# Kernel optimization log

Hardware: AMD Instinct MI355X
Metric: run time of the kernel (lower is better)

Reference implementation:

```python
import jax, jax.numpy as jnp
import numpy as np
import math

B, S, E, H, F, L, V = 4, 256, 512, 8, 2048, 4, 32000
HD = E // H
MAXLEN = 5000  # EnhancedPositionalEncoding max_len default


def _ln(x, s, b):
    m = jnp.mean(x, axis=-1, keepdims=True)
    v = jnp.mean((x - m) ** 2, axis=-1, keepdims=True)
    return (x - m) / jnp.sqrt(v + 1e-5) * s + b


def setup_inputs() -> dict:
    key = jax.random.key(0)
    ks = jax.random.split(key, 10)
    n = lambda k, shape: jax.random.normal(k, shape, jnp.float32) * 0.02
    return {
        "src": jax.random.randint(ks[0], (B, S), 0, V),
        "emb": jax.random.uniform(ks[1], (V, E), jnp.float32, -0.1, 0.1),
        "rel_table": n(ks[2], (2 * MAXLEN - 1, E)),
        "norm_in_s": jnp.ones(E, jnp.float32), "norm_in_b": jnp.zeros(E, jnp.float32),
        "inW": n(ks[3], (L, 3 * E, E)), "inB": jnp.zeros((L, 3 * E), jnp.float32),
        "outW": n(ks[4], (L, E, E)), "outB": jnp.zeros((L, E), jnp.float32),
        "ln1_s": jnp.ones((L, E), jnp.float32), "ln1_b": jnp.zeros((L, E), jnp.float32),
        "ln2_s": jnp.ones((L, E), jnp.float32), "ln2_b": jnp.zeros((L, E), jnp.float32),
        "w1": n(ks[5], (L, F, E)), "b1": jnp.zeros((L, F), jnp.float32),
        "w2": n(ks[6], (L, E, F)), "b2": jnp.zeros((L, E), jnp.float32),
        "normf_s": jnp.ones(E, jnp.float32), "normf_b": jnp.zeros(E, jnp.float32),
        "dec_w": jax.random.uniform(ks[7], (V, E), jnp.float32, -0.1, 0.1),
        "dec_b": jnp.zeros(V, jnp.float32),
    }


def reference(src, emb, rel_table, norm_in_s, norm_in_b, inW, inB, outW, outB,
              ln1_s, ln1_b, ln2_s, ln2_b, w1, b1, w2, b2, normf_s, normf_b,
              dec_w, dec_b):
    x = emb[src] * math.sqrt(E)                 # [B,S,E], pos_encoder is identity in relative mode
    x = _ln(x, norm_in_s, norm_in_b)
    # relative-position embedding gather: idx[l,m] = (m - l) + S - 1
    pos = jnp.arange(S)
    rel_idx = (pos[None, :] - pos[:, None]) + S - 1
    rel = rel_table[rel_idx].reshape(S, S, H, HD)  # [S,S,H,hd]
    # NOTE: torch adds the BOOL triu mask to float scores -> +1.0 at masked positions
    mask = jnp.triu(jnp.ones((S, S), jnp.float32), 1)
    scale = 1.0 / math.sqrt(HD)
    for l in range(L):
        h = _ln(x, ln1_s[l], ln1_b[l])
        qkv = h @ inW[l].T + inB[l]
        q, k, v = jnp.split(qkv, 3, axis=-1)
        q = q.reshape(B, S, H, HD).transpose(0, 2, 1, 3)  # [B,H,S,hd]
        k = k.reshape(B, S, H, HD).transpose(0, 2, 1, 3)
        v = v.reshape(B, S, H, HD).transpose(0, 2, 1, 3)
        scores = jnp.einsum('bhqd,bhkd->bhqk', q, k) * scale
        bias = jnp.einsum('bhld,lmhd->bhlm', q, rel)      # relative-position bias (unscaled, as in torch)
        attn = jax.nn.softmax(scores + bias + mask, axis=-1)
        o = jnp.einsum('bhqk,bhkd->bhqd', attn, v).transpose(0, 2, 1, 3).reshape(B, S, E)
        x = x + (o @ outW[l].T + outB[l])
        h2 = _ln(x, ln2_s[l], ln2_b[l])
        ff = jax.nn.gelu(h2 @ w1[l].T + b1[l], approximate=False) @ w2[l].T + b2[l]
        x = x + ff
    x = _ln(x, normf_s, normf_b)  # encoder final norm
    return x @ dec_w.T + dec_b    # [B,S,V]
```

## Files before the change

### kernel.cpp

```cpp
#include <hip/hip_runtime.h>
#include <hip/hip_bf16.h>
#include <math.h>

#define BB 4
#define SS 256
#define EE 512
#define HH 8
#define HD 64
#define FFD 2048
#define LL 4
#define VV 32000
#define BS (BB*SS)
#define SQRT_E 22.627416997969522f
#define ATTN_SCALE 0.125f

typedef __bf16 bf16;
typedef __attribute__((ext_vector_type(4))) __bf16 bf16x4;
typedef __attribute__((ext_vector_type(8))) __bf16 bf16x8;
typedef __attribute__((ext_vector_type(4))) float f32x4;

#define GLOBAL_AS __attribute__((address_space(1)))
#define LDS_AS    __attribute__((address_space(3)))

__device__ __forceinline__ void load_lds16(const bf16* g, bf16* l) {
    __builtin_amdgcn_global_load_lds((const GLOBAL_AS unsigned int*)g,
                                     (LDS_AS unsigned int*)l, 16, 0, 0);
}

__global__ void cvt_all(const float* __restrict__ inW, const float* __restrict__ outW,
                        const float* __restrict__ w1, const float* __restrict__ w2,
                        const float* __restrict__ dec, const float* __restrict__ rel,
                        bf16* __restrict__ inWb, bf16* __restrict__ outWb,
                        bf16* __restrict__ w1b, bf16* __restrict__ w2b,
                        bf16* __restrict__ decb, bf16* __restrict__ relb) {
    int b = blockIdx.x;
    const float* s; bf16* d; int base; int n;
    if (b < 3072)       { s = inW;  d = inWb;  base = b;         n = 3145728; }
    else if (b < 4096)  { s = outW; d = outWb; base = b - 3072;  n = 1048576; }
    else if (b < 8192)  { s = w1;   d = w1b;   base = b - 4096;  n = 4194304; }
    else if (b < 12288) { s = w2;   d = w2b;   base = b - 8192;  n = 4194304; }
    else if (b < 28288) { s = dec;  d = decb;  base = b - 12288; n = 16384000; }
    else                { s = rel;  d = relb;  base = b - 28288; n = 261632; }
    int i = (base * 256 + threadIdx.x) * 4;
    if (i < n) {
        float4 v = *(const float4*)(s + i);
        bf16x4 o;
        o[0] = (bf16)v.x; o[1] = (bf16)v.y; o[2] = (bf16)v.z; o[3] = (bf16)v.w;
        *(bf16x4*)(d + i) = o;
    }
}

template <typename OT>
__global__ void ln_kernel(const float* __restrict__ in, const float* __restrict__ sc,
                          const float* __restrict__ bi, OT* __restrict__ out) {
    int row = blockIdx.x;
    int t = threadIdx.x;
    const float* r = in + (size_t)row * EE;
    float v0 = r[t], v1 = r[t + 256];
    float sum = v0 + v1, sq = v0 * v0 + v1 * v1;
    #pragma unroll
    for (int off = 32; off; off >>= 1) {
        sum += __shfl_xor(sum, off);
        sq  += __shfl_xor(sq, off);
    }
    __shared__ float ssum[4], ssq[4];
    int wid = t >> 6, lane = t & 63;
    if (lane == 0) { ssum[wid] = sum; ssq[wid] = sq; }
    __syncthreads();
    sum = ssum[0] + ssum[1] + ssum[2] + ssum[3];
    sq  = ssq[0] + ssq[1] + ssq[2] + ssq[3];
    float mean = sum * (1.0f / EE);
    float var  = sq * (1.0f / EE) - mean * mean;
    float rstd = rsqrtf(var + 1e-5f);
    out[(size_t)row * EE + t]       = (OT)((v0 - mean) * rstd * sc[t] + bi[t]);
    out[(size_t)row * EE + t + 256] = (OT)((v1 - mean) * rstd * sc[t + 256] + bi[t + 256]);
}

__global__ void embed_ln_kernel(const int* __restrict__ src, const float* __restrict__ emb,
                                const float* __restrict__ sc, const float* __restrict__ bi,
                                float* __restrict__ out) {
    int row = blockIdx.x;
    int t = threadIdx.x;
    const float* r = emb + (size_t)src[row] * EE;
    float v0 = r[t] * SQRT_E, v1 = r[t + 256] * SQRT_E;
    float sum = v0 + v1, sq = v0 * v0 + v1 * v1;
    #pragma unroll
    for (int off = 32; off; off >>= 1) {
        sum += __shfl_xor(sum, off);
        sq  += __shfl_xor(sq, off);
    }
    __shared__ float ssum[4], ssq[4];
    int wid = t >> 6, lane = t & 63;
    if (lane == 0) { ssum[wid] = sum; ssq[wid] = sq; }
    __syncthreads();
    sum = ssum[0] + ssum[1] + ssum[2] + ssum[3];
    sq  = ssq[0] + ssq[1] + ssq[2] + ssq[3];
    float mean = sum * (1.0f / EE);
    float var  = sq * (1.0f / EE) - mean * mean;
    float rstd = rsqrtf(var + 1e-5f);
    out[(size_t)row * EE + t]       = (v0 - mean) * rstd * sc[t] + bi[t];
    out[(size_t)row * EE + t + 256] = (v1 - mean) * rstd * sc[t + 256] + bi[t + 256];
}

template <int BM, int BN, int MODE, int OBF16, int WRVT, int SWZ>
__global__ __launch_bounds__(256) void gemm_bf16(
        const bf16* __restrict__ A, const bf16* __restrict__ W,
        const float* __restrict__ bias, void* __restrict__ Cout,
        const float* __restrict__ res, bf16* __restrict__ vT,
        int M, int N, int K) {
    constexpr int FM = BM / 32, FN = BN / 32;
    __shared__ bf16 Atile[2][BM * 32];
    __shared__ bf16 Btile[2][BN * 32];
    int tid = threadIdx.x;
    int wid = tid >> 6, lane = tid & 63;
    int wm = (wid >> 1) * (BM / 2), wn = (wid & 1) * (BN / 2);
    int bm, bn;
    if (SWZ) {
        int nbm = gridDim.x;
        int linear = blockIdx.y * nbm + blockIdx.x;
        int total = nbm * gridDim.y;
        int chunk = total >> 3;
        int xcd = linear & 7, idx = linear >> 3;
        int g = xcd * chunk + idx;
        bm = (g % nbm) * BM;
        bn = (g / nbm) * BN;
    } else {
        bm = blockIdx.x * BM;
        bn = blockIdx.y * BN;
    }

    f32x4 acc[FM][FN];
    #pragma unroll
    for (int i = 0; i < FM; i++)
        #pragma unroll
        for (int j = 0; j < FN; j++)
            acc[i][j] = (f32x4){0.f, 0.f, 0.f, 0.f};

    int mrow = lane & 15, kq = (lane >> 4) * 8;

    auto stage = [&](int buf, int k0) {
        #pragma unroll
        for (int it = 0; it < BM / 64; it++) {
            int c = it * 256 + tid;
            int row = c >> 2, kc = (c & 3) * 8;
            load_lds16(A + (size_t)(bm + row) * K + k0 + kc, &Atile[buf][c * 8]);
        }
        #pragma unroll
        for (int it = 0; it < BN / 64; it++) {
            int c = it * 256 + tid;
            int row = c >> 2, kc = (c & 3) * 8;
            load_lds16(W + (size_t)(bn + row) * K + k0 + kc, &Btile[buf][c * 8]);
        }
    };

    stage(0, 0);
    __syncthreads();
    int cur = 0;
    for (int k0 = 0; k0 < K; k0 += 32) {
        if (k0 + 32 < K) stage(cur ^ 1, k0 + 32);
        bf16x8 af[FM], bfv[FN];
        #pragma unroll
        for (int i = 0; i < FM; i++)
            af[i] = *(const bf16x8*)(&Atile[cur][(wm + i * 16 + mrow) * 32 + kq]);
        #pragma unroll
        for (int j = 0; j < FN; j++)
            bfv[j] = *(const bf16x8*)(&Btile[cur][(wn + j * 16 + mrow) * 32 + kq]);
        #pragma unroll
        for (int i = 0; i < FM; i++)
            #pragma unroll
            for (int j = 0; j < FN; j++)
                acc[i][j] = __builtin_amdgcn_mfma_f32_16x16x32_bf16(af[i], bfv[j], acc[i][j], 0, 0, 0);
        __syncthreads();
        cur ^= 1;
    }

    #pragma unroll
    for (int i = 0; i < FM; i++) {
        int row0 = bm + wm + i * 16 + (lane >> 4) * 4;
        #pragma unroll
        for (int j = 0; j < FN; j++) {
            int col = bn + wn + j * 16 + (lane & 15);
            float bv = bias[col];
            #pragma unroll
            for (int r = 0; r < 4; r++) {
                int row = row0 + r;
                float v = acc[i][j][r] + bv;
                if (MODE == 1) v = 0.5f * v * (1.0f + erff(v * 0.7071067811865476f));
                if (MODE == 2) v += res[(size_t)row * N + col];
                if (WRVT && col >= 1024) {
                    int cc = col - 1024;
                    vT[(size_t)(((row >> 8) * 8 + (cc >> 6)) * 64 + (cc & 63)) * 256 + (row & 255)] = (bf16)v;
                } else if (OBF16) ((bf16*)Cout)[(size_t)row * N + col] = (bf16)v;
                else              ((float*)Cout)[(size_t)row * N + col] = v;
            }
        }
    }
}

__global__ __launch_bounds__(256) void attn_mfma(const bf16* __restrict__ qkv,
        const bf16* __restrict__ relb, const bf16* __restrict__ vT,
        bf16* __restrict__ o) {
    int blk = blockIdx.x;
    int qt = blk & 3, bh = blk >> 2;
    int h = bh & 7, b = bh >> 3;
    int q0 = qt * 64, j0 = 192 - q0;
    int tid = threadIdx.x;
    int wid = tid >> 6, lane = tid & 63;
    int l15 = lane & 15, quad = lane >> 4;
    int mr0 = wid * 16;

    __shared__ __align__(16) bf16 Qs[64 * 72];
    __shared__ __align__(16) bf16 Stg[64 * 72];
    __shared__ __align__(16) bf16 BP[64 * 264];

    int c0 = tid, c1 = 256 + tid;
    int r0 = c0 >> 3, ch0 = (c0 & 7) * 8;
    int r1 = c1 >> 3, ch1 = (c1 & 7) * 8;

    const size_t qbase = (size_t)(b * 256 + q0) * 1536 + h * 64;
    *(bf16x8*)(Qs + r0 * 72 + ch0) = *(const bf16x8*)(qkv + qbase + (size_t)r0 * 1536 + ch0);
    *(bf16x8*)(Qs + r1 * 72 + ch1) = *(const bf16x8*)(qkv + qbase + (size_t)r1 * 1536 + ch1);

    bf16x8 pf0, pf1;
    {
        const size_t rb = (size_t)j0 * 512 + h * 64;
        pf0 = *(const bf16x8*)(relb + rb + (size_t)r0 * 512 + ch0);
        pf1 = *(const bf16x8*)(relb + rb + (size_t)r1 * 512 + ch1);
    }

    __syncthreads();
    bf16x8 af0 = *(const bf16x8*)(Qs + (mr0 + l15) * 72 + quad * 8);
    bf16x8 af1 = *(const bf16x8*)(Qs + (mr0 + l15) * 72 + 32 + quad * 8);

    f32x4 S[16];
    #pragma unroll
    for (int i = 0; i < 16; i++) S[i] = (f32x4){0.f, 0.f, 0.f, 0.f};

    for (int jc = 0; jc < 5; jc++) {
        *(bf16x8*)(Stg + r0 * 72 + ch0) = pf0;
        *(bf16x8*)(Stg + r1 * 72 + ch1) = pf1;
        __syncthreads();
        if (jc < 4) {
            const size_t rb = (size_t)(j0 + (jc + 1) * 64) * 512 + h * 64;
            pf0 = *(const bf16x8*)(relb + rb + (size_t)r0 * 512 + ch0);
            pf1 = *(const bf16x8*)(relb + rb + (size_t)r1 * 512 + ch1);
        } else {
            const size_t kb = (size_t)(b * 256) * 1536 + 512 + h * 64;
            pf0 = *(const bf16x8*)(qkv + kb + (size_t)r0 * 1536 + ch0);
            pf1 = *(const bf16x8*)(qkv + kb + (size_t)r1 * 1536 + ch1);
        }
        #pragma unroll
        for (int jt = 0; jt < 4; jt++) {
            f32x4 acc = (f32x4){0.f, 0.f, 0.f, 0.f};
            bf16x8 bv0 = *(const bf16x8*)(Stg + (jt * 16 + l15) * 72 + quad * 8);
            bf16x8 bv1 = *(const bf16x8*)(Stg + (jt * 16 + l15) * 72 + 32 + quad * 8);
            acc = __builtin_amdgcn_mfma_f32_16x16x32_bf16(af0, bv0, acc, 0, 0, 0);
            acc = __builtin_amdgcn_mfma_f32_16x16x32_bf16(af1, bv1, acc, 0, 0, 0);
            int jp = jc * 64 + jt * 16 + l15;
            #pragma unroll
            for (int r = 0; r < 4; r++) {
                int ll = mr0 + quad * 4 + r;
                int m = jp + ll - 63;
                if (m >= 0 && m < 256) BP[ll * 256 + m] = (bf16)acc[r];
            }
        }
        __syncthreads();
    }

    for (int kc = 0; kc < 4; kc++) {
        *(bf16x8*)(Stg + r0 * 72 + ch0) = pf0;
        *(bf16x8*)(Stg + r1 * 72 + ch1) = pf1;
        __syncthreads();
        if (kc < 3) {
            const size_t kb = (size_t)(b * 256 + (kc + 1) * 64) * 1536 + 512 + h * 64;
            pf0 = *(const bf16x8*)(qkv + kb + (size_t)r0 * 1536 + ch0);
            pf1 = *(const bf16x8*)(qkv + kb + (size_t)r1 * 1536 + ch1);
        } else {
            const size_t vb = (size_t)(bh * 64) * 256;
            pf0 = *(const bf16x8*)(vT + vb + (size_t)r0 * 256 + ch0);
            pf1 = *(const bf16x8*)(vT + vb + (size_t)r1 * 256 + ch1);
        }
        #pragma unroll
        for (int nt = 0; nt < 4; nt++) {
            bf16x8 bv0 = *(const bf16x8*)(Stg + (nt * 16 + l15) * 72 + quad * 8);
            bf16x8 bv1 = *(const bf16x8*)(Stg + (nt * 16 + l15) * 72 + 32 + quad * 8);
            S[kc * 4 + nt] = __builtin_amdgcn_mfma_f32_16x16x32_bf16(af0, bv0, S[kc * 4 + nt], 0, 0, 0);
            S[kc * 4 + nt] = __builtin_amdgcn_mfma_f32_16x16x32_bf16(af1, bv1, S[kc * 4 + nt], 0, 0, 0);
        }
        __syncthreads();
    }

    float rmax[4] = {-1e30f, -1e30f, -1e30f, -1e30f};
    #pragma unroll
    for (int T = 0; T < 16; T++) {
        int m = T * 16 + l15;
        #pragma unroll
        for (int r = 0; r < 4; r++) {
            int ll = mr0 + quad * 4 + r;
            float v = S[T][r] * ATTN_SCALE + (float)BP[ll * 256 + m]
                      + ((m > q0 + ll) ? 1.0f : 0.0f);
            S[T][r] = v;
            rmax[r] = fmaxf(rmax[r], v);
        }
    }
    #pragma unroll
    for (int r = 0; r < 4; r++)
        #pragma unroll
        for (int d = 1; d < 16; d <<= 1)
            rmax[r] = fmaxf(rmax[r], __shfl_xor(rmax[r], d));
    float rsum[4] = {0.f, 0.f, 0.f, 0.f};
    #pragma unroll
    for (int T = 0; T < 16; T++)
        #pragma unroll
        for (int r = 0; r < 4; r++) {
            float p = expf(S[T][r] - rmax[r]);
            S[T][r] = p;
            rsum[r] += p;
        }
    #pragma unroll
    for (int r = 0; r < 4; r++)
        #pragma unroll
        for (int d = 1; d < 16; d <<= 1)
            rsum[r] += __shfl_xor(rsum[r], d);

    __syncthreads();
    #pragma unroll
    for (int T = 0; T < 16; T++)
        #pragma unroll
        for (int r = 0; r < 4; r++)
            BP[(mr0 + quad * 4 + r) * 264 + T * 16 + l15] = (bf16)S[T][r];

    f32x4 oacc[4];
    #pragma unroll
    for (int i = 0; i < 4; i++) oacc[i] = (f32x4){0.f, 0.f, 0.f, 0.f};
    for (int kc = 0; kc < 4; kc++) {
        *(bf16x8*)(Stg + r0 * 72 + ch0) = pf0;
        *(bf16x8*)(Stg + r1 * 72 + ch1) = pf1;
        __syncthreads();
        if (kc < 3) {
            const size_t vb = (size_t)(bh * 64) * 256 + (kc + 1) * 64;
            pf0 = *(const bf16x8*)(vT + vb + (size_t)r0 * 256 + ch0);
            pf1 = *(const bf16x8*)(vT + vb + (size_t)r1 * 256 + ch1);
        }
        #pragma unroll
        for (int ks = 0; ks < 2; ks++) {
            bf16x8 ap = *(const bf16x8*)(BP + (mr0 + l15) * 264 + kc * 64 + ks * 32 + quad * 8);
            #pragma unroll
            for (int nt = 0; nt < 4; nt++) {
                bf16x8 bv = *(const bf16x8*)(Stg + (nt * 16 + l15) * 72 + ks * 32 + quad * 8);
                oacc[nt] = __builtin_amdgcn_mfma_f32_16x16x32_bf16(ap, bv, oacc[nt], 0, 0, 0);
            }
        }
        __syncthreads();
    }

    #pragma unroll
    for (int nt = 0; nt < 4; nt++)
        #pragma unroll
        for (int r = 0; r < 4; r++) {
            int ll = mr0 + quad * 4 + r;
            o[(size_t)(b * 256 + q0 + ll) * 512 + h * 64 + nt * 16 + l15] =
                (bf16)(oacc[nt][r] * (1.0f / rsum[r]));
        }
}

template <int MODE>
__global__ void gemm_nt(const float* __restrict__ A, const float* __restrict__ W,
                        const float* __restrict__ bias, float* __restrict__ C,
                        const float* __restrict__ res, int M, int N, int K) {
    __shared__ float As[64][17];
    __shared__ float Ws[64][17];
    int tid = threadIdx.x;
    int tx = tid & 15, ty = tid >> 4;
    int bm = blockIdx.y * 64, bn = blockIdx.x * 64;
    float acc[4][4] = {};
    for (int k0 = 0; k0 < K; k0 += 16) {
        #pragma unroll
        for (int i = 0; i < 4; i++) {
            int idx = tid + i * 256;
            int r = idx >> 4, c = idx & 15;
            As[r][c] = A[(size_t)(bm + r) * K + k0 + c];
            Ws[r][c] = W[(size_t)(bn + r) * K + k0 + c];
        }
        __syncthreads();
        #pragma unroll
        for (int kk = 0; kk < 16; kk++) {
            float a[4], w[4];
            #pragma unroll
            for (int i = 0; i < 4; i++) a[i] = As[ty * 4 + i][kk];
            #pragma unroll
            for (int j = 0; j < 4; j++) w[j] = Ws[tx * 4 + j][kk];
            #pragma unroll
            for (int i = 0; i < 4; i++)
                #pragma unroll
                for (int j = 0; j < 4; j++)
                    acc[i][j] += a[i] * w[j];
        }
        __syncthreads();
    }
    #pragma unroll
    for (int i = 0; i < 4; i++) {
        int row = bm + ty * 4 + i;
        #pragma unroll
        for (int j = 0; j < 4; j++) {
            int col = bn + tx * 4 + j;
            float v = acc[i][j] + bias[col];
            if (MODE == 1) v = 0.5f * v * (1.0f + erff(v * 0.7071067811865476f));
            if (MODE == 2) v += res[(size_t)row * N + col];
            C[(size_t)row * N + col] = v;
        }
    }
}

__global__ void attn_kernel(const float* __restrict__ qkv, const float* __restrict__ rel_table,
                            float* __restrict__ o) {
    int blk = blockIdx.x;
    int l = blk & (SS - 1);
    int bh = blk >> 8;
    int h = bh & (HH - 1);
    int b = bh >> 3;
    int t = threadIdx.x;
    int wid = t >> 6, lane = t & 63;

    __shared__ float qs[HD];
    __shared__ float attn_s[SS];
    __shared__ float swave[4];
    __shared__ float opart[4][HD];

    const float* qrow = qkv + (size_t)(b * SS + l) * (3 * EE) + h * HD;
    if (t < HD) qs[t] = qrow[t];
    __syncthreads();

    const float* krow   = qkv + (size_t)(b * SS + t) * (3 * EE) + EE + h * HD;
    const float* relrow = rel_table + (size_t)(t - l + SS - 1) * EE + h * HD;
    const float4* k4 = reinterpret_cast<const float4*>(krow);
    const float4* r4 = reinterpret_cast<const float4*>(relrow);
    float s1 = 0.f, s2 = 0.f;
    #pragma unroll
    for (int d4 = 0; d4 < HD / 4; d4++) {
        float4 kv = k4[d4], rv = r4[d4];
        float q0 = qs[4 * d4], q1 = qs[4 * d4 + 1], q2 = qs[4 * d4 + 2], q3 = qs[4 * d4 + 3];
        s1 += q0 * kv.x + q1 * kv.y + q2 * kv.z + q3 * kv.w;
        s2 += q0 * rv.x + q1 * rv.y + q2 * rv.z + q3 * rv.w;
    }
    float val = s1 * ATTN_SCALE + s2 + ((t > l) ? 1.0f : 0.0f);

    float m = val;
    #pragma unroll
    for (int off = 32; off; off >>= 1) m = fmaxf(m, __shfl_xor(m, off));
    if (lane == 0) swave[wid] = m;
    __syncthreads();
    m = fmaxf(fmaxf(swave[0], swave[1]), fmaxf(swave[2], swave[3]));
    float p = expf(val - m);
    float s = p;
    #pragma unroll
    for (int off = 32; off; off >>= 1) s += __shfl_xor(s, off);
    __syncthreads();
    if (lane == 0) swave[wid] = s;
    __syncthreads();
    float tot = swave[0] + swave[1] + swave[2] + swave[3];
    attn_s[t] = p;
    __syncthreads();

    int d = t & 63, part = t >> 6;
    const float* vbase = qkv + (size_t)(b * SS) * (3 * EE) + 2 * EE + h * HD + d;
    float acc = 0.f;
    int m0 = part * 64;
    #pragma unroll 8
    for (int mm = m0; mm < m0 + 64; mm++)
        acc += attn_s[mm] * vbase[(size_t)mm * (3 * EE)];
    opart[part][d] = acc;
    __syncthreads();
    if (t < 64) {
        float ov = (opart[0][d] + opart[1][d] + opart[2][d] + opart[3][d]) / tot;
        o[(size_t)(b * SS + l) * EE + h * HD + d] = ov;
    }
}

extern "C" void kernel_launch(void* const* d_in, const int* in_sizes, int n_in,
                              void* d_out, int out_size, void* d_ws, size_t ws_size,
                              hipStream_t stream) {
    const int*   src    = (const int*)  d_in[0];
    const float* emb    = (const float*)d_in[1];
    const float* rel    = (const float*)d_in[2];
    const float* nin_s  = (const float*)d_in[3];
    const float* nin_b  = (const float*)d_in[4];
    const float* inW    = (const float*)d_in[5];
    const float* inB    = (const float*)d_in[6];
    const float* outW   = (const float*)d_in[7];
    const float* outB   = (const float*)d_in[8];
    const float* ln1_s  = (const float*)d_in[9];
    const float* ln1_b  = (const float*)d_in[10];
    const float* ln2_s  = (const float*)d_in[11];
    const float* ln2_b  = (const float*)d_in[12];
    const float* w1     = (const float*)d_in[13];
    const float* b1     = (const float*)d_in[14];
    const float* w2     = (const float*)d_in[15];
    const float* b2     = (const float*)d_in[16];
    const float* normf_s= (const float*)d_in[17];
    const float* normf_b= (const float*)d_in[18];
    const float* dec_w  = (const float*)d_in[19];
    const float* dec_b  = (const float*)d_in[20];
    float* out = (float*)d_out;

    const size_t n_inW  = (size_t)LL * 3 * EE * EE;
    const size_t n_outW = (size_t)LL * EE * EE;
    const size_t n_w1   = (size_t)LL * FFD * EE;
    const size_t n_w2   = (size_t)LL * EE * FFD;
    const size_t n_dec  = (size_t)VV * EE;

    float* x    = (float*)d_ws;
    bf16*  qkvb = (bf16*)(x + (size_t)BS * EE);
    bf16*  hb   = qkvb + (size_t)BS * 3 * EE;
    bf16*  ob   = hb + (size_t)BS * EE;
    bf16*  ffb  = ob + (size_t)BS * EE;
    bf16*  vTb  = ffb + (size_t)BS * FFD;
    bf16*  relb = vTb + (size_t)BS * 512;
    bf16*  inWb  = relb + (size_t)512 * EE;
    bf16*  outWb = inWb + n_inW;
    bf16*  w1b   = outWb + n_outW;
    bf16*  w2b   = w1b + n_w1;
    bf16*  decWb = w2b + n_w2;
    size_t needed = (size_t)((char*)(decWb + n_dec) - (char*)d_ws);

    if (ws_size >= needed) {
        embed_ln_kernel<<<BS, 256, 0, stream>>>(src, emb, nin_s, nin_b, x);
        cvt_all<<<28544, 256, 0, stream>>>(inW, outW, w1, w2, dec_w, rel,
                                           inWb, outWb, w1b, w2b, decWb, relb);

        for (int l = 0; l < LL; l++) {
            ln_kernel<bf16><<<BS, 256, 0, stream>>>(x, ln1_s + l * EE, ln1_b + l * EE, hb);
            gemm_bf16<64, 64, 0, 1, 1, 0><<<dim3(BS / 64, 3 * EE / 64), 256, 0, stream>>>(
                hb, inWb + (size_t)l * 3 * EE * EE, inB + (size_t)l * 3 * EE, qkvb, nullptr,
                vTb, BS, 3 * EE, EE);
            attn_mfma<<<BB * HH * 4, 256, 0, stream>>>(qkvb, relb, vTb, ob);
            gemm_bf16<64, 64, 2, 0, 0, 0><<<dim3(BS / 64, EE / 64), 256, 0, stream>>>(
                ob, outWb + (size_t)l * EE * EE, outB + (size_t)l * EE, x, x,
                nullptr, BS, EE, EE);
            ln_kernel<bf16><<<BS, 256, 0, stream>>>(x, ln2_s + l * EE, ln2_b + l * EE, hb);
            gemm_bf16<64, 64, 1, 1, 0, 0><<<dim3(BS / 64, FFD / 64), 256, 0, stream>>>(
                hb, w1b + (size_t)l * FFD * EE, b1 + (size_t)l * FFD, ffb, nullptr,
                nullptr, BS, FFD, EE);
            gemm_bf16<64, 64, 2, 0, 0, 0><<<dim3(BS / 64, EE / 64), 256, 0, stream>>>(
                ffb, w2b + (size_t)l * EE * FFD, b2 + (size_t)l * EE, x, x,
                nullptr, BS, EE, FFD);
        }

        ln_kernel<bf16><<<BS, 256, 0, stream>>>(x, normf_s, normf_b, hb);
        gemm_bf16<128, 128, 0, 0, 0, 1><<<dim3(BS / 128, VV / 128), 256, 0, stream>>>(
            hb, decWb, dec_b, out, nullptr, nullptr, BS, VV, EE);
    } else {
        float* h     = x + (size_t)BS * EE;
        float* qkvf  = h + (size_t)BS * EE;
        float* o     = qkvf + (size_t)BS * 3 * EE;
        float* ffmid = o + (size_t)BS * EE;

        embed_ln_kernel<<<BS, 256, 0, stream>>>(src, emb, nin_s, nin_b, x);
        for (int l = 0; l < LL; l++) {
            ln_kernel<float><<<BS, 256, 0, stream>>>(x, ln1_s + l * EE, ln1_b + l * EE, h);
            gemm_nt<0><<<dim3(3 * EE / 64, BS / 64), 256, 0, stream>>>(
                h, inW + (size_t)l * 3 * EE * EE, inB + (size_t)l * 3 * EE, qkvf, nullptr,
                BS, 3 * EE, EE);
            attn_kernel<<<BB * HH * SS, 256, 0, stream>>>(qkvf, rel, o);
            gemm_nt<2><<<dim3(EE / 64, BS / 64), 256, 0, stream>>>(
                o, outW + (size_t)l * EE * EE, outB + (size_t)l * EE, x, x,
                BS, EE, EE);
            ln_kernel<float><<<BS, 256, 0, stream>>>(x, ln2_s + l * EE, ln2_b + l * EE, h);
            gemm_nt<1><<<dim3(FFD / 64, BS / 64), 256, 0, stream>>>(
                h, w1 + (size_t)l * FFD * EE, b1 + (size_t)l * FFD, ffmid, nullptr,
                BS, FFD, EE);
            gemm_nt<2><<<dim3(EE / 64, BS / 64), 256, 0, stream>>>(
                ffmid, w2 + (size_t)l * EE * FFD, b2 + (size_t)l * EE, x, x,
                BS, EE, FFD);
        }
        ln_kernel<float><<<BS, 256, 0, stream>>>(x, normf_s, normf_b, h);
        gemm_nt<0><<<dim3(VV / 64, BS / 64), 256, 0, stream>>>(
            h, dec_w, dec_b, out, nullptr, BS, VV, EE);
    }
}
```

Before: 621.7 us.

## Fuse layernorm into GEMM A-loads, widen BK with swizzled LDS, merge embed into convert

Per-layer LayerNorms before the QKV and FFN1 GEMMs are folded into the GEMM: each block computes row mean/rstd from the fp32 residual, then loads fp32 A through registers, normalizes, converts to bf16 and stores it into LDS. The GEMM gains a BK template parameter (64 for layer GEMMs) with XOR-swizzled LDS slots to reduce bank conflicts. The output-projection and FFN2 GEMMs use 32x64 tiles to launch more blocks, and the embedding+LN kernel is merged into the weight-conversion launch. This removes two LN launches and the bf16 h round trip per layer, at the cost of redundant row-statistics work per N-block and register-staged A loads instead of direct global-to-LDS loads.

```diff
diff --git a/kernel.cpp b/kernel.cpp
--- a/kernel.cpp
+++ b/kernel.cpp
@@ -32,8 +32,35 @@
                         const float* __restrict__ dec, const float* __restrict__ rel,
                         bf16* __restrict__ inWb, bf16* __restrict__ outWb,
                         bf16* __restrict__ w1b, bf16* __restrict__ w2b,
-                        bf16* __restrict__ decb, bf16* __restrict__ relb) {
+                        bf16* __restrict__ decb, bf16* __restrict__ relb,
+                        const int* __restrict__ src, const float* __restrict__ emb,
+                        const float* __restrict__ nsc, const float* __restrict__ nbi,
+                        float* __restrict__ xout) {
     int b = blockIdx.x;
+    int t = threadIdx.x;
+    if (b >= 28544) {
+        int row = b - 28544;
+        const float* r = emb + (size_t)src[row] * EE;
+        float v0 = r[t] * SQRT_E, v1 = r[t + 256] * SQRT_E;
+        float sum = v0 + v1, sq = v0 * v0 + v1 * v1;
+        #pragma unroll
+        for (int off = 32; off; off >>= 1) {
+            sum += __shfl_xor(sum, off);
+            sq  += __shfl_xor(sq, off);
+        }
+        __shared__ float ssum[4], ssq[4];
+        int wid = t >> 6, lane = t & 63;
+        if (lane == 0) { ssum[wid] = sum; ssq[wid] = sq; }
+        __syncthreads();
+        sum = ssum[0] + ssum[1] + ssum[2] + ssum[3];
+        sq  = ssq[0] + ssq[1] + ssq[2] + ssq[3];
+        float mean = sum * (1.0f / EE);
+        float var  = sq * (1.0f / EE) - mean * mean;
+        float rstd = rsqrtf(var + 1e-5f);
+        xout[(size_t)row * EE + t]       = (v0 - mean) * rstd * nsc[t] + nbi[t];
+        xout[(size_t)row * EE + t + 256] = (v1 - mean) * rstd * nsc[t + 256] + nbi[t + 256];
+        return;
+    }
     const float* s; bf16* d; int base; int n;
     if (b < 3072)       { s = inW;  d = inWb;  base = b;         n = 3145728; }
     else if (b < 4096)  { s = outW; d = outWb; base = b - 3072;  n = 1048576; }
@@ -41,7 +68,7 @@
     else if (b < 12288) { s = w2;   d = w2b;   base = b - 8192;  n = 4194304; }
     else if (b < 28288) { s = dec;  d = decb;  base = b - 12288; n = 16384000; }
     else                { s = rel;  d = relb;  base = b - 28288; n = 261632; }
-    int i = (base * 256 + threadIdx.x) * 4;
+    int i = (base * 256 + t) * 4;
     if (i < n) {
         float4 v = *(const float4*)(s + i);
         bf16x4 o;
@@ -102,18 +129,26 @@
     out[(size_t)row * EE + t + 256] = (v1 - mean) * rstd * sc[t + 256] + bi[t + 256];
 }
 
-template <int BM, int BN, int MODE, int OBF16, int WRVT, int SWZ>
+template <int BM, int BN, int BK, int MODE, int OBF16, int WRVT, int SWZ, int LNF>
 __global__ __launch_bounds__(256) void gemm_bf16(
-        const bf16* __restrict__ A, const bf16* __restrict__ W,
-        const float* __restrict__ bias, void* __restrict__ Cout,
-        const float* __restrict__ res, bf16* __restrict__ vT,
-        int M, int N, int K) {
+        const bf16* __restrict__ A, const float* __restrict__ Xf,
+        const float* __restrict__ lnsc, const float* __restrict__ lnbi,
+        const bf16* __restrict__ W, const float* __restrict__ bias,
+        void* __restrict__ Cout, const float* __restrict__ res,
+        bf16* __restrict__ vT, int M, int N, int K) {
     constexpr int FM = BM / 32, FN = BN / 32;
-    __shared__ bf16 Atile[2][BM * 32];
-    __shared__ bf16 Btile[2][BN * 32];
+    constexpr int KSTEPS = BK / 32;
+    constexpr int SLOTS = BK / 8;
+    constexpr int SWZM = SLOTS - 1;
+    constexpr int NA = BM * BK / 2048;
+    constexpr int NB = BN * BK / 2048;
+    __shared__ __align__(16) bf16 Atile[2][BM * BK];
+    __shared__ __align__(16) bf16 Btile[2][BN * BK];
+    __shared__ float lnm[LNF ? BM : 1], lnr[LNF ? BM : 1];
     int tid = threadIdx.x;
     int wid = tid >> 6, lane = tid & 63;
     int wm = (wid >> 1) * (BM / 2), wn = (wid & 1) * (BN / 2);
+    int mrow = lane & 15, quad = lane >> 4;
     int bm, bn;
     if (SWZ) {
         int nbm = gridDim.x;
@@ -129,6 +164,28 @@
         bn = blockIdx.y * BN;
     }
 
+    if (LNF) {
+        constexpr int TPR = 256 / BM;
+        constexpr int CPT = EE / TPR;
+        int row = tid / TPR, sub = tid % TPR;
+        const float* xr = Xf + (size_t)(bm + row) * EE + sub * CPT;
+        float sum = 0.f, sq = 0.f;
+        #pragma unroll
+        for (int j = 0; j < CPT; j += 4) {
+            float4 v = *(const float4*)(xr + j);
+            sum += v.x + v.y + v.z + v.w;
+            sq  += v.x * v.x + v.y * v.y + v.z * v.z + v.w * v.w;
+        }
+        #pragma unroll
+        for (int d = 1; d < TPR; d <<= 1) { sum += __shfl_xor(sum, d); sq += __shfl_xor(sq, d); }
+        if (sub == 0) {
+            float mean = sum * (1.0f / EE);
+            float var  = sq * (1.0f / EE) - mean * mean;
+            lnm[row] = mean; lnr[row] = rsqrtf(var + 1e-5f);
+        }
+        __syncthreads();
+    }
+
     f32x4 acc[FM][FN];
     #pragma unroll
     for (int i = 0; i < FM; i++)
@@ -136,50 +193,101 @@
         for (int j = 0; j < FN; j++)
             acc[i][j] = (f32x4){0.f, 0.f, 0.f, 0.f};
 
-    int mrow = lane & 15, kq = (lane >> 4) * 8;
-
-    auto stage = [&](int buf, int k0) {
-        #pragma unroll
-        for (int it = 0; it < BM / 64; it++) {
-            int c = it * 256 + tid;
-            int row = c >> 2, kc = (c & 3) * 8;
+    float4 apre[NA][2];
+    auto aload = [&](int k0) {
+        #pragma unroll
+        for (int s = 0; s < NA; s++) {
+            int c = s * 256 + tid; int row = c / SLOTS; int slot = c % SLOTS;
+            int kc = (slot ^ (row & SWZM)) * 8;
+            const float* p = Xf + (size_t)(bm + row) * K + k0 + kc;
+            apre[s][0] = *(const float4*)p;
+            apre[s][1] = *(const float4*)(p + 4);
+        }
+    };
+    auto astore = [&](int buf, int k0) {
+        #pragma unroll
+        for (int s = 0; s < NA; s++) {
+            int c = s * 256 + tid; int row = c / SLOTS; int slot = c % SLOTS;
+            int kc = (slot ^ (row & SWZM)) * 8;
+            float mean = lnm[row], rstd = lnr[row];
+            float4 s0 = *(const float4*)(lnsc + k0 + kc);
+            float4 s1 = *(const float4*)(lnsc + k0 + kc + 4);
+            float4 b0 = *(const float4*)(lnbi + k0 + kc);
+            float4 b1 = *(const float4*)(lnbi + k0 + kc + 4);
+            bf16x8 o;
+            o[0] = (bf16)((apre[s][0].x - mean) * rstd * s0.x + b0.x);
+            o[1] = (bf16)((apre[s][0].y - mean) * rstd * s0.y + b0.y);
+            o[2] = (bf16)((apre[s][0].z - mean) * rstd * s0.z + b0.z);
+            o[3] = (bf16)((apre[s][0].w - mean) * rstd * s0.w + b0.w);
+            o[4] = (bf16)((apre[s][1].x - mean) * rstd * s1.x + b1.x);
+            o[5] = (bf16)((apre[s][1].y - mean) * rstd * s1.y + b1.y);
+            o[6] = (bf16)((apre[s][1].z - mean) * rstd * s1.z + b1.z);
+            o[7] = (bf16)((apre[s][1].w - mean) * rstd * s1.w + b1.w);
+            *(bf16x8*)(&Atile[buf][c * 8]) = o;
+        }
+    };
+    auto stageA = [&](int buf, int k0) {
+        #pragma unroll
+        for (int s = 0; s < NA; s++) {
+            int c = s * 256 + tid; int row = c / SLOTS; int slot = c % SLOTS;
+            int kc = (slot ^ (row & SWZM)) * 8;
             load_lds16(A + (size_t)(bm + row) * K + k0 + kc, &Atile[buf][c * 8]);
         }
-        #pragma unroll
-        for (int it = 0; it < BN / 64; it++) {
-            int c = it * 256 + tid;
-            int row = c >> 2, kc = (c & 3) * 8;
+    };
+    auto stageB = [&](int buf, int k0) {
+        #pragma unroll
+        for (int s = 0; s < NB; s++) {
+            int c = s * 256 + tid; int row = c / SLOTS; int slot = c % SLOTS;
+            int kc = (slot ^ (row & SWZM)) * 8;
             load_lds16(W + (size_t)(bn + row) * K + k0 + kc, &Btile[buf][c * 8]);
         }
     };
 
-    stage(0, 0);
+    if (LNF) { aload(0); astore(0, 0); } else stageA(0, 0);
+    stageB(0, 0);
     __syncthreads();
     int cur = 0;
-    for (int k0 = 0; k0 < K; k0 += 32) {
-        if (k0 + 32 < K) stage(cur ^ 1, k0 + 32);
-        bf16x8 af[FM], bfv[FN];
+    for (int k0 = 0; k0 < K; k0 += BK) {
+        bool next = (k0 + BK < K);
+        if (next) {
+            if (LNF) aload(k0 + BK); else stageA(cur ^ 1, k0 + BK);
+            stageB(cur ^ 1, k0 + BK);
+        }
+        bf16x8 af[FM][KSTEPS], bfv[FN][KSTEPS];
         #pragma unroll
         for (int i = 0; i < FM; i++)
-            af[i] = *(const bf16x8*)(&Atile[cur][(wm + i * 16 + mrow) * 32 + kq]);
+            #pragma unroll
+            for (int ks = 0; ks < KSTEPS; ks++) {
+                int row = wm + i * 16 + mrow;
+                int slot = ks * 4 + quad;
+                af[i][ks] = *(const bf16x8*)(&Atile[cur][row * BK + ((slot ^ (row & SWZM)) * 8)]);
+            }
         #pragma unroll
         for (int j = 0; j < FN; j++)
-            bfv[j] = *(const bf16x8*)(&Btile[cur][(wn + j * 16 + mrow) * 32 + kq]);
-        #pragma unroll
-        for (int i = 0; i < FM; i++)
-            #pragma unroll
-            for (int j = 0; j < FN; j++)
-                acc[i][j] = __builtin_amdgcn_mfma_f32_16x16x32_bf16(af[i], bfv[j], acc[i][j], 0, 0, 0);
+            #pragma unroll
+            for (int ks = 0; ks < KSTEPS; ks++) {
+                int row = wn + j * 16 + mrow;
+                int slot = ks * 4 + quad;
+                bfv[j][ks] = *(const bf16x8*)(&Btile[cur][row * BK + ((slot ^ (row & SWZM)) * 8)]);
+            }
+        #pragma unroll
+        for (int ks = 0; ks < KSTEPS; ks++)
+            #pragma unroll
+            for (int i = 0; i < FM; i++)
+                #pragma unroll
+                for (int j = 0; j < FN; j++)
+                    acc[i][j] = __builtin_amdgcn_mfma_f32_16x16x32_bf16(af[i][ks], bfv[j][ks], acc[i][j], 0, 0, 0);
+        if (LNF && next) astore(cur ^ 1, k0 + BK);
         __syncthreads();
         cur ^= 1;
     }
 
     #pragma unroll
     for (int i = 0; i < FM; i++) {
-        int row0 = bm + wm + i * 16 + (lane >> 4) * 4;
+        int row0 = bm + wm + i * 16 + quad * 4;
         #pragma unroll
         for (int j = 0; j < FN; j++) {
-            int col = bn + wn + j * 16 + (lane & 15);
+            int col = bn + wn + j * 16 + mrow;
             float bv = bias[col];
             #pragma unroll
             for (int r = 0; r < 4; r++) {
@@ -524,31 +632,33 @@
     size_t needed = (size_t)((char*)(decWb + n_dec) - (char*)d_ws);
 
     if (ws_size >= needed) {
-        embed_ln_kernel<<<BS, 256, 0, stream>>>(src, emb, nin_s, nin_b, x);
-        cvt_all<<<28544, 256, 0, stream>>>(inW, outW, w1, w2, dec_w, rel,
-                                           inWb, outWb, w1b, w2b, decWb, relb);
+        cvt_all<<<29568, 256, 0, stream>>>(inW, outW, w1, w2, dec_w, rel,
+                                           inWb, outWb, w1b, w2b, decWb, relb,
+                                           src, emb, nin_s, nin_b, x);
 
         for (int l = 0; l < LL; l++) {
-            ln_kernel<bf16><<<BS, 256, 0, stream>>>(x, ln1_s + l * EE, ln1_b + l * EE, hb);
-            gemm_bf16<64, 64, 0, 1, 1, 0><<<dim3(BS / 64, 3 * EE / 64), 256, 0, stream>>>(
-                hb, inWb + (size_t)l * 3 * EE * EE, inB + (size_t)l * 3 * EE, qkvb, nullptr,
-                vTb, BS, 3 * EE, EE);
+            gemm_bf16<64, 64, 64, 0, 1, 1, 0, 1><<<dim3(BS / 64, 3 * EE / 64), 256, 0, stream>>>(
+                nullptr, x, ln1_s + (size_t)l * EE, ln1_b + (size_t)l * EE,
+                inWb + (size_t)l * 3 * EE * EE, inB + (size_t)l * 3 * EE,
+                qkvb, nullptr, vTb, BS, 3 * EE, EE);
             attn_mfma<<<BB * HH * 4, 256, 0, stream>>>(qkvb, relb, vTb, ob);
-            gemm_bf16<64, 64, 2, 0, 0, 0><<<dim3(BS / 64, EE / 64), 256, 0, stream>>>(
-                ob, outWb + (size_t)l * EE * EE, outB + (size_t)l * EE, x, x,
-                nullptr, BS, EE, EE);
-            ln_kernel<bf16><<<BS, 256, 0, stream>>>(x, ln2_s + l * EE, ln2_b + l * EE, hb);
-            gemm_bf16<64, 64, 1, 1, 0, 0><<<dim3(BS / 64, FFD / 64), 256, 0, stream>>>(
-                hb, w1b + (size_t)l * FFD * EE, b1 + (size_t)l * FFD, ffb, nullptr,
-                nullptr, BS, FFD, EE);
-            gemm_bf16<64, 64, 2, 0, 0, 0><<<dim3(BS / 64, EE / 64), 256, 0, stream>>>(
-                ffb, w2b + (size_t)l * EE * FFD, b2 + (size_t)l * EE, x, x,
-                nullptr, BS, EE, FFD);
+            gemm_bf16<32, 64, 64, 2, 0, 0, 0, 0><<<dim3(BS / 32, EE / 64), 256, 0, stream>>>(
+                ob, nullptr, nullptr, nullptr,
+                outWb + (size_t)l * EE * EE, outB + (size_t)l * EE,
+                x, x, nullptr, BS, EE, EE);
+            gemm_bf16<64, 64, 64, 1, 1, 0, 0, 1><<<dim3(BS / 64, FFD / 64), 256, 0, stream>>>(
+                nullptr, x, ln2_s + (size_t)l * EE, ln2_b + (size_t)l * EE,
+                w1b + (size_t)l * FFD * EE, b1 + (size_t)l * FFD,
+                ffb, nullptr, nullptr, BS, FFD, EE);
+            gemm_bf16<32, 64, 64, 2, 0, 0, 0, 0><<<dim3(BS / 32, EE / 64), 256, 0, stream>>>(
+                ffb, nullptr, nullptr, nullptr,
+                w2b + (size_t)l * EE * FFD, b2 + (size_t)l * EE,
+                x, x, nullptr, BS, EE, FFD);
         }
 
         ln_kernel<bf16><<<BS, 256, 0, stream>>>(x, normf_s, normf_b, hb);
-        gemm_bf16<128, 128, 0, 0, 0, 1><<<dim3(BS / 128, VV / 128), 256, 0, stream>>>(
-            hb, decWb, dec_b, out, nullptr, nullptr, BS, VV, EE);
+        gemm_bf16<128, 128, 32, 0, 0, 0, 1, 0><<<dim3(BS / 128, VV / 128), 256, 0, stream>>>(
+            hb, nullptr, nullptr, nullptr, decWb, dec_b, out, nullptr, nullptr, BS, VV, EE);
     } else {
         float* h     = x + (size_t)BS * EE;
         float* qkvf  = h + (size_t)BS * EE;
```

After: 658.4 us. +5.9%, slower.

## Split-K with atomic accumulation for residual GEMMs; fuse embed-LN into convert kernel

Applied to the files above, without the earlier changes.

The out-projection and FFN-down GEMMs, which have only 128 tiles each, now use split-K (2 and 4 ways). Partial sums are atomically added straight into the residual buffer x, so the residual add falls out of the in-place accumulation. Separately, the embedding+layernorm kernel is merged into the weight-conversion launch as extra blocks, which saves one launch. The atomics add contention and make the summation order nondeterministic, but they give more parallelism on a GPU with many compute units.

```diff
diff --git a/kernel.cpp b/kernel.cpp
--- a/kernel.cpp
+++ b/kernel.cpp
@@ -32,8 +32,35 @@
                         const float* __restrict__ dec, const float* __restrict__ rel,
                         bf16* __restrict__ inWb, bf16* __restrict__ outWb,
                         bf16* __restrict__ w1b, bf16* __restrict__ w2b,
-                        bf16* __restrict__ decb, bf16* __restrict__ relb) {
+                        bf16* __restrict__ decb, bf16* __restrict__ relb,
+                        const int* __restrict__ src, const float* __restrict__ emb,
+                        const float* __restrict__ nsc, const float* __restrict__ nbi,
+                        float* __restrict__ xout) {
     int b = blockIdx.x;
+    int t = threadIdx.x;
+    if (b >= 28544) {
+        int row = b - 28544;
+        const float* r = emb + (size_t)src[row] * EE;
+        float v0 = r[t] * SQRT_E, v1 = r[t + 256] * SQRT_E;
+        float sum = v0 + v1, sq = v0 * v0 + v1 * v1;
+        #pragma unroll
+        for (int off = 32; off; off >>= 1) {
+            sum += __shfl_xor(sum, off);
+            sq  += __shfl_xor(sq, off);
+        }
+        __shared__ float ssum[4], ssq[4];
+        int wid = t >> 6, lane = t & 63;
+        if (lane == 0) { ssum[wid] = sum; ssq[wid] = sq; }
+        __syncthreads();
+        sum = ssum[0] + ssum[1] + ssum[2] + ssum[3];
+        sq  = ssq[0] + ssq[1] + ssq[2] + ssq[3];
+        float mean = sum * (1.0f / EE);
+        float var  = sq * (1.0f / EE) - mean * mean;
+        float rstd = rsqrtf(var + 1e-5f);
+        xout[(size_t)row * EE + t]       = (v0 - mean) * rstd * nsc[t] + nbi[t];
+        xout[(size_t)row * EE + t + 256] = (v1 - mean) * rstd * nsc[t + 256] + nbi[t + 256];
+        return;
+    }
     const float* s; bf16* d; int base; int n;
     if (b < 3072)       { s = inW;  d = inWb;  base = b;         n = 3145728; }
     else if (b < 4096)  { s = outW; d = outWb; base = b - 3072;  n = 1048576; }
@@ -41,7 +68,7 @@
     else if (b < 12288) { s = w2;   d = w2b;   base = b - 8192;  n = 4194304; }
     else if (b < 28288) { s = dec;  d = decb;  base = b - 12288; n = 16384000; }
     else                { s = rel;  d = relb;  base = b - 28288; n = 261632; }
-    int i = (base * 256 + threadIdx.x) * 4;
+    int i = (base * 256 + t) * 4;
     if (i < n) {
         float4 v = *(const float4*)(s + i);
         bf16x4 o;
@@ -102,7 +129,7 @@
     out[(size_t)row * EE + t + 256] = (v1 - mean) * rstd * sc[t + 256] + bi[t + 256];
 }
 
-template <int BM, int BN, int MODE, int OBF16, int WRVT, int SWZ>
+template <int BM, int BN, int MODE, int OBF16, int WRVT, int SWZ, int SPLITK>
 __global__ __launch_bounds__(256) void gemm_bf16(
         const bf16* __restrict__ A, const bf16* __restrict__ W,
         const float* __restrict__ bias, void* __restrict__ Cout,
@@ -128,6 +155,9 @@
         bm = blockIdx.x * BM;
         bn = blockIdx.y * BN;
     }
+    int kp = (SPLITK > 1) ? blockIdx.z : 0;
+    int kbeg = kp * (K / SPLITK);
+    int kend = kbeg + K / SPLITK;
 
     f32x4 acc[FM][FN];
     #pragma unroll
@@ -153,11 +183,11 @@
         }
     };
 
-    stage(0, 0);
+    stage(0, kbeg);
     __syncthreads();
     int cur = 0;
-    for (int k0 = 0; k0 < K; k0 += 32) {
-        if (k0 + 32 < K) stage(cur ^ 1, k0 + 32);
+    for (int k0 = kbeg; k0 < kend; k0 += 32) {
+        if (k0 + 32 < kend) stage(cur ^ 1, k0 + 32);
         bf16x8 af[FM], bfv[FN];
         #pragma unroll
         for (int i = 0; i < FM; i++)
@@ -184,6 +214,12 @@
             #pragma unroll
             for (int r = 0; r < 4; r++) {
                 int row = row0 + r;
+                if (SPLITK > 1) {
+                    float v = acc[i][j][r];
+                    if (kp == 0) v += bv;
+                    atomicAdd((float*)Cout + (size_t)row * N + col, v);
+                    continue;
+                }
                 float v = acc[i][j][r] + bv;
                 if (MODE == 1) v = 0.5f * v * (1.0f + erff(v * 0.7071067811865476f));
                 if (MODE == 2) v += res[(size_t)row * N + col];
@@ -524,30 +560,30 @@
     size_t needed = (size_t)((char*)(decWb + n_dec) - (char*)d_ws);
 
     if (ws_size >= needed) {
-        embed_ln_kernel<<<BS, 256, 0, stream>>>(src, emb, nin_s, nin_b, x);
-        cvt_all<<<28544, 256, 0, stream>>>(inW, outW, w1, w2, dec_w, rel,
-                                           inWb, outWb, w1b, w2b, decWb, relb);
+        cvt_all<<<29568, 256, 0, stream>>>(inW, outW, w1, w2, dec_w, rel,
+                                           inWb, outWb, w1b, w2b, decWb, relb,
+                                           src, emb, nin_s, nin_b, x);
 
         for (int l = 0; l < LL; l++) {
             ln_kernel<bf16><<<BS, 256, 0, stream>>>(x, ln1_s + l * EE, ln1_b + l * EE, hb);
-            gemm_bf16<64, 64, 0, 1, 1, 0><<<dim3(BS / 64, 3 * EE / 64), 256, 0, stream>>>(
+            gemm_bf16<64, 64, 0, 1, 1, 0, 1><<<dim3(BS / 64, 3 * EE / 64), 256, 0, stream>>>(
                 hb, inWb + (size_t)l * 3 * EE * EE, inB + (size_t)l * 3 * EE, qkvb, nullptr,
                 vTb, BS, 3 * EE, EE);
             attn_mfma<<<BB * HH * 4, 256, 0, stream>>>(qkvb, relb, vTb, ob);
-            gemm_bf16<64, 64, 2, 0, 0, 0><<<dim3(BS / 64, EE / 64), 256, 0, stream>>>(
+            gemm_bf16<64, 64, 2, 0, 0, 0, 2><<<dim3(BS / 64, EE / 64, 2), 256, 0, stream>>>(
                 ob, outWb + (size_t)l * EE * EE, outB + (size_t)l * EE, x, x,
                 nullptr, BS, EE, EE);
             ln_kernel<bf16><<<BS, 256, 0, stream>>>(x, ln2_s + l * EE, ln2_b + l * EE, hb);
-            gemm_bf16<64, 64, 1, 1, 0, 0><<<dim3(BS / 64, FFD / 64), 256, 0, stream>>>(
+            gemm_bf16<64, 64, 1, 1, 0, 0, 1><<<dim3(BS / 64, FFD / 64), 256, 0, stream>>>(
                 hb, w1b + (size_t)l * FFD * EE, b1 + (size_t)l * FFD, ffb, nullptr,
                 nullptr, BS, FFD, EE);
-            gemm_bf16<64, 64, 2, 0, 0, 0><<<dim3(BS / 64, EE / 64), 256, 0, stream>>>(
+            gemm_bf16<64, 64, 2, 0, 0, 0, 4><<<dim3(BS / 64, EE / 64, 4), 256, 0, stream>>>(
                 ffb, w2b + (size_t)l * EE * FFD, b2 + (size_t)l * EE, x, x,
                 nullptr, BS, EE, FFD);
         }
 
         ln_kernel<bf16><<<BS, 256, 0, stream>>>(x, normf_s, normf_b, hb);
-        gemm_bf16<128, 128, 0, 0, 0, 1><<<dim3(BS / 128, VV / 128), 256, 0, stream>>>(
+        gemm_bf16<128, 128, 0, 0, 0, 1, 1><<<dim3(BS / 128, VV / 128), 256, 0, stream>>>(
             hb, decWb, dec_b, out, nullptr, nullptr, BS, VV, EE);
     } else {
         float* h     = x + (size_t)BS * EE;
```

Result: faster. 577.2 us (-7.2%).
